# Performance work log

Hardware: AMD Instinct MI355X
Metric: run time of the kernel (lower is better)

The kernel has to match this reference:

```python
import jax, jax.numpy as jnp
import numpy as np

B, S, I, H, L1, O = 128, 1024, 256, 512, 256, 64

def _xavier(key, shape):
    fan_in, fan_out = shape[-2] if len(shape) > 1 else shape[-1], shape[-1]
    limit = float(np.sqrt(6.0 / (fan_in + fan_out)))
    return jax.random.uniform(key, shape, jnp.float32, -limit, limit)

def setup_inputs() -> dict:
    key = jax.random.key(0)
    ks = jax.random.split(key, 20)
    d = {"X": jax.random.normal(ks[0], (B, S, I), jnp.float32)}
    names = [("W_xi", (I, H)), ("W_hi", (H, H)), ("b_i", (1, H)),
             ("W_xf", (I, H)), ("W_hf", (H, H)), ("b_f", (1, H)),
             ("W_xo", (I, H)), ("W_ho", (H, H)), ("b_o", (1, H)),
             ("W_xc", (I, H)), ("W_hc", (H, H)), ("b_c", (1, H)),
             ("W_o1", (H, L1)), ("b_o1", (1, L1)), ("W_o2", (L1, O)), ("b_o2", (1, O))]
    for k, (n, shp) in zip(ks[1:], names):
        d[n] = _xavier(k, shp)
    return d

def reference(X, W_xi, W_hi, b_i, W_xf, W_hf, b_f, W_xo, W_ho, b_o, W_xc, W_hc, b_c, W_o1, b_o1, W_o2, b_o2):
    batch = X.shape[0]
    hid = W_hi.shape[0]
    # Precompute all input projections in one big GEMM: [B,S,4H]
    Wx = jnp.concatenate([W_xi, W_xf, W_xo, W_xc], axis=1)
    pre = jnp.einsum('bsi,ig->bsg', X, Wx)  # [B,S,4H]
    pre = jnp.transpose(pre, (1, 0, 2))     # [S,B,4H] for scan

    def step(carry, p):
        Hs, Cs = carry
        pi, pf, po, pc = jnp.split(p, 4, axis=-1)
        Ig = jax.nn.sigmoid(pi + Hs @ W_hi + b_i)
        Fg = jax.nn.sigmoid(pf + Hs @ W_hf + b_f)
        Og = jax.nn.sigmoid(po + Hs @ W_ho + b_o)
        Ct = jnp.tanh(pc + Hs @ W_hc + b_c)
        Cn = Fg * Cs + Ig * Ct
        # NOTE: original module uses tanh(C) + O (addition), not O * tanh(C)
        Hn = jnp.tanh(Cn) + Og
        return (Hn, Cn), None

    H0 = jnp.zeros((batch, hid), X.dtype)
    C0 = jnp.zeros((batch, hid), X.dtype)
    (Hf, Cf), _ = jax.lax.scan(step, (H0, C0), pre)
    # Output head: only the final timestep's output is returned by the loop
    h1 = jax.nn.relu(Hf @ W_o1 + b_o1)
    output = jax.nn.softmax(h1 @ W_o2 + b_o2, axis=1)
    return output, Hf, Cf
```

## Files before the change

kernel.cpp:

```cpp
#include <hip/hip_runtime.h>

#define B_   128
#define S_   1024
#define I_   256
#define H_   512
#define L1_  256
#define O_   64

#define NGRP 8
#define WGPG 32
#define MB   16
#define NH   16
#define NCOL 64
#define SX   8
#define SH   16

#define HB_UINTS_PER_BUF 32768

typedef __attribute__((ext_vector_type(8))) short short8;
typedef __attribute__((ext_vector_type(4))) float f4;
typedef __attribute__((ext_vector_type(4))) unsigned u32x4;

__device__ __forceinline__ unsigned short f2bf(float x) {
  unsigned u = __builtin_bit_cast(unsigned, x);
  u += 0x7FFFu + ((u >> 16) & 1u);
  return (unsigned short)(u >> 16);
}

__device__ __forceinline__ f4 mfma_bf16(short8 a, short8 b, f4 c) {
  asm("v_mfma_f32_16x16x32_bf16 %0, %1, %2, %0" : "+v"(c) : "v"(a), "v"(b));
  return c;
}

__global__ __launch_bounds__(256, 1)
void lstm_rec(const float* __restrict__ X,
              const float* __restrict__ Wxi, const float* __restrict__ Whi, const float* __restrict__ bi,
              const float* __restrict__ Wxf, const float* __restrict__ Whf, const float* __restrict__ bfp,
              const float* __restrict__ Wxo, const float* __restrict__ Who, const float* __restrict__ bop,
              const float* __restrict__ Wxc, const float* __restrict__ Whc, const float* __restrict__ bcp,
              float* __restrict__ out, unsigned* __restrict__ flags, unsigned* __restrict__ Hbuf)
{
  __shared__ unsigned short WhF[4][SH][64][8];
  __shared__ unsigned short WxF[4][SX][64][8];
  __shared__ unsigned short As[SX + SH][64][8];
  __shared__ float Ps[MB][NCOL];
  __shared__ float bias_s[NCOL];
  __shared__ int go_s;

  const int tid  = threadIdx.x;
  const int lane = tid & 63;
  const int wv   = tid >> 6;
  const int g    = blockIdx.x & 7;
  const int jg   = blockIdx.x >> 3;
  const int j0   = jg * NH;
  const int b0   = g * MB;

  const float* Whg[4] = {Whi, Whf, Who, Whc};
  const float* Wxg[4] = {Wxi, Wxf, Wxo, Wxc};
  const float* bg[4]  = {bi, bfp, bop, bcp};

  for (int gate = 0; gate < 4; ++gate) {
    const float* Wp = Whg[gate];
    for (int it = 0; it < 32; ++it) {
      int idx = it * 256 + tid;
      int k = idx >> 4, c = idx & 15;
      WhF[gate][k >> 5][((k & 31) >> 3) * 16 + c][k & 7] = f2bf(Wp[(size_t)k * H_ + j0 + c]);
    }
    const float* Xp = Wxg[gate];
    for (int it = 0; it < 16; ++it) {
      int idx = it * 256 + tid;
      int k = idx >> 4, c = idx & 15;
      WxF[gate][k >> 5][((k & 31) >> 3) * 16 + c][k & 7] = f2bf(Xp[(size_t)k * H_ + j0 + c]);
    }
  }
  if (tid < NCOL) bias_s[tid] = bg[tid >> 4][j0 + (tid & 15)];
  if (tid == 0) go_s = 0;
  __syncthreads();

  float Creg = 0.f;
  const int pb = tid >> 4;
  const int ph = tid & 15;
  unsigned* myflags = flags + g * 32;

  for (int t = 0; t < S_; ++t) {
    #pragma unroll
    for (int it = 0; it < 2; ++it) {
      int idx = it * 256 + tid;
      int s = idx >> 6, pos = idx & 63;
      int row = pos & 15, k0 = s * 32 + (pos >> 4) * 8;
      const float* src = X + ((size_t)(b0 + row) * S_ + t) * I_ + k0;
      float4 v0 = *(const float4*)(src);
      float4 v1 = *(const float4*)(src + 4);
      union { unsigned short us[8]; u32x4 v; } pk;
      pk.us[0] = f2bf(v0.x); pk.us[1] = f2bf(v0.y); pk.us[2] = f2bf(v0.z); pk.us[3] = f2bf(v0.w);
      pk.us[4] = f2bf(v1.x); pk.us[5] = f2bf(v1.y); pk.us[6] = f2bf(v1.z); pk.us[7] = f2bf(v1.w);
      *(u32x4*)&As[s][pos][0] = pk.v;
    }
    __syncthreads();

    float bv = bias_s[wv * 16 + (lane & 15)];
    f4 acc = {bv, bv, bv, bv};
    asm("s_nop 1" : "+v"(acc));
    #pragma unroll
    for (int s = 0; s < SX; ++s) {
      short8 a = *(const short8*)&As[s][lane][0];
      short8 b = *(const short8*)&WxF[wv][s][lane][0];
      acc = mfma_bf16(a, b, acc);
    }

    if (t > 0) {
      if (wv == 0) {
        const unsigned target = (unsigned)t;
        for (;;) {
          unsigned v = __hip_atomic_load(myflags + (lane & 31),
                                         __ATOMIC_RELAXED, __HIP_MEMORY_SCOPE_AGENT);
          if (__all(v >= target)) break;
          __builtin_amdgcn_s_sleep(1);
        }
        if (lane == 0) *(volatile int*)&go_s = t;
      } else {
        while (*(volatile int*)&go_s < t) __builtin_amdgcn_s_sleep(1);
      }
      const u32x4* gp = (const u32x4*)(Hbuf + (size_t)(t & 1) * HB_UINTS_PER_BUF + g * 4096);
      u32x4 r0, r1, r2, r3;
      asm volatile(
        "global_load_dwordx4 %0, %4, off sc0 sc1\n\t"
        "global_load_dwordx4 %1, %5, off sc0 sc1\n\t"
        "global_load_dwordx4 %2, %6, off sc0 sc1\n\t"
        "global_load_dwordx4 %3, %7, off sc0 sc1\n\t"
        "s_waitcnt vmcnt(0)"
        : "=&v"(r0), "=&v"(r1), "=&v"(r2), "=&v"(r3)
        : "v"(gp + tid), "v"(gp + tid + 256), "v"(gp + tid + 512), "v"(gp + tid + 768)
        : "memory");
      u32x4* lp = (u32x4*)&As[SX][0][0];
      lp[tid]       = r0;
      lp[tid + 256] = r1;
      lp[tid + 512] = r2;
      lp[tid + 768] = r3;
    }
    __syncthreads();

    if (t > 0) {
      #pragma unroll
      for (int s = 0; s < SH; ++s) {
        short8 a = *(const short8*)&As[SX + s][lane][0];
        short8 b = *(const short8*)&WhF[wv][s][lane][0];
        acc = mfma_bf16(a, b, acc);
      }
    }
    asm("s_nop 7\n\ts_nop 7" : "+v"(acc));
    {
      int col = wv * 16 + (lane & 15);
      int r0 = (lane >> 4) * 4;
      Ps[r0 + 0][col] = acc[0];
      Ps[r0 + 1][col] = acc[1];
      Ps[r0 + 2][col] = acc[2];
      Ps[r0 + 3][col] = acc[3];
    }
    __syncthreads();

    {
      float pi = Ps[pb][ph];
      float pf = Ps[pb][16 + ph];
      float po = Ps[pb][32 + ph];
      float pc = Ps[pb][48 + ph];
      float Ig = 1.f / (1.f + __expf(-pi));
      float Fg = 1.f / (1.f + __expf(-pf));
      float Og = 1.f / (1.f + __expf(-po));
      float Ct = 1.f - 2.f / (__expf(2.f * pc) + 1.f);
      float Cn = Fg * Creg + Ig * Ct;
      Creg = Cn;
      float Hn = (1.f - 2.f / (__expf(2.f * Cn) + 1.f)) + Og;
      if (t < S_ - 1) {
        unsigned hb = f2bf(Hn);
        unsigned other = (unsigned)__shfl_xor((int)hb, 1, 64);
        if ((ph & 1) == 0) {
          unsigned packed = hb | (other << 16);
          int sl = jg >> 1;
          int pos = ((jg & 1) * 2 + (ph >> 3)) * 16 + pb;
          unsigned* dst = Hbuf + (size_t)((t + 1) & 1) * HB_UINTS_PER_BUF + g * 4096
                        + (sl * 64 + pos) * 4 + ((ph & 7) >> 1);
          __hip_atomic_store(dst, packed, __ATOMIC_RELAXED, __HIP_MEMORY_SCOPE_AGENT);
        }
      } else {
        out[B_ * O_ + (size_t)(b0 + pb) * H_ + j0 + ph] = Hn;
        out[B_ * O_ + B_ * H_ + (size_t)(b0 + pb) * H_ + j0 + ph] = Cn;
      }
    }
    if (t < S_ - 1) {
      __syncthreads();
      if (tid == 0)
        __hip_atomic_store(myflags + jg, (unsigned)(t + 1),
                           __ATOMIC_RELAXED, __HIP_MEMORY_SCOPE_AGENT);
    }
  }
}

__global__ __launch_bounds__(256, 1)
void lstm_head(const float* __restrict__ Hf,
               const float* __restrict__ Wo1, const float* __restrict__ bo1,
               const float* __restrict__ Wo2, const float* __restrict__ bo2,
               float* __restrict__ outp)
{
  __shared__ float hf[H_];
  __shared__ float h1[L1_];
  const int tid = threadIdx.x;
  const int b = blockIdx.x;
  hf[tid]       = Hf[(size_t)b * H_ + tid];
  hf[tid + 256] = Hf[(size_t)b * H_ + tid + 256];
  __syncthreads();
  float a = bo1[tid];
  #pragma unroll 8
  for (int k = 0; k < H_; ++k) a = fmaf(hf[k], Wo1[(size_t)k * L1_ + tid], a);
  h1[tid] = fmaxf(a, 0.f);
  __syncthreads();
  if (tid < O_) {
    float l = bo2[tid];
    #pragma unroll 8
    for (int j = 0; j < L1_; ++j) l = fmaf(h1[j], Wo2[(size_t)j * O_ + tid], l);
    float m = l;
    #pragma unroll
    for (int off = 32; off > 0; off >>= 1) m = fmaxf(m, __shfl_xor(m, off, 64));
    float e = __expf(l - m);
    float ssum = e;
    #pragma unroll
    for (int off = 32; off > 0; off >>= 1) ssum += __shfl_xor(ssum, off, 64);
    outp[(size_t)b * O_ + tid] = e / ssum;
  }
}

extern "C" void kernel_launch(void* const* d_in, const int* in_sizes, int n_in,
                              void* d_out, int out_size, void* d_ws, size_t ws_size,
                              hipStream_t stream) {
  (void)in_sizes; (void)n_in; (void)out_size; (void)ws_size;
  const float* X   = (const float*)d_in[0];
  const float* Wxi = (const float*)d_in[1];
  const float* Whi = (const float*)d_in[2];
  const float* bi  = (const float*)d_in[3];
  const float* Wxf = (const float*)d_in[4];
  const float* Whf = (const float*)d_in[5];
  const float* bfv = (const float*)d_in[6];
  const float* Wxo = (const float*)d_in[7];
  const float* Who = (const float*)d_in[8];
  const float* bo  = (const float*)d_in[9];
  const float* Wxc = (const float*)d_in[10];
  const float* Whc = (const float*)d_in[11];
  const float* bc  = (const float*)d_in[12];
  const float* Wo1 = (const float*)d_in[13];
  const float* bo1 = (const float*)d_in[14];
  const float* Wo2 = (const float*)d_in[15];
  const float* bo2 = (const float*)d_in[16];
  float* out = (float*)d_out;

  unsigned* flags = (unsigned*)d_ws;
  unsigned* Hbuf  = (unsigned*)((char*)d_ws + 1024);

  hipMemsetAsync(d_ws, 0, 1024, stream);
  hipLaunchKernelGGL(lstm_rec, dim3(NGRP * WGPG), dim3(256), 0, stream,
                     X, Wxi, Whi, bi, Wxf, Whf, bfv, Wxo, Who, bo, Wxc, Whc, bc,
                     out, flags, Hbuf);
  hipLaunchKernelGGL(lstm_head, dim3(B_), dim3(256), 0, stream,
                     out + B_ * O_, Wo1, bo1, Wo2, bo2, out);
}
```

Measured before the change: 2.703 ms.

## Prefetch next X step, keep weights in registers, pick XCC-local cache scope

The X slice for step t+1 is now loaded into registers during step t and written to a double-buffered LDS area that reuses the WxF storage, taking the X load latency off the critical path. The Wx and Wh MFMA operand fragments are also held in registers, so the per-step LDS reads of weights go away. A startup handshake records each workgroup's XCC ID. When all workgroups in a batch group share one XCC, the H exchange uses sc0-only loads and stores so it can stay in the local L2 rather than going to system scope. The flag poll is issued early, before the Wx MFMAs, to hide its latency. The costs are much higher register pressure, extra startup synchronisation, and reliance on same-XCC coherence being correct.

```diff
diff --git a/kernel.cpp b/kernel.cpp
--- a/kernel.cpp
+++ b/kernel.cpp
@@ -38,14 +38,16 @@
               const float* __restrict__ Wxf, const float* __restrict__ Whf, const float* __restrict__ bfp,
               const float* __restrict__ Wxo, const float* __restrict__ Who, const float* __restrict__ bop,
               const float* __restrict__ Wxc, const float* __restrict__ Whc, const float* __restrict__ bcp,
-              float* __restrict__ out, unsigned* __restrict__ flags, unsigned* __restrict__ Hbuf)
+              float* __restrict__ out, unsigned* __restrict__ flags,
+              unsigned* __restrict__ xslots, unsigned* __restrict__ Hbuf)
 {
   __shared__ unsigned short WhF[4][SH][64][8];
   __shared__ unsigned short WxF[4][SX][64][8];
-  __shared__ unsigned short As[SX + SH][64][8];
+  __shared__ unsigned short AsH[SH][64][8];
   __shared__ float Ps[MB][NCOL];
   __shared__ float bias_s[NCOL];
   __shared__ int go_s;
+  __shared__ int mode_s;
 
   const int tid  = threadIdx.x;
   const int lane = tid & 63;
@@ -55,6 +57,25 @@
   const int j0   = jg * NH;
   const int b0   = g * MB;
 
+  unsigned xcc;
+  asm volatile("s_getreg_b32 %0, hwreg(HW_REG_XCC_ID)" : "=s"(xcc));
+  xcc &= 15u;
+  if (tid == 0)
+    __hip_atomic_store(xslots + g * 32 + jg, xcc + 1u,
+                       __ATOMIC_RELAXED, __HIP_MEMORY_SCOPE_AGENT);
+
+  const int idxA = tid, idxB = 256 + tid;
+  const int sA = idxA >> 6, posA = idxA & 63;
+  const int sB = idxB >> 6, posB = idxB & 63;
+  const int offA = (sA * 64 + posA) * 8;
+  const int offB = (sB * 64 + posB) * 8;
+  const float* bpa = X + (size_t)(b0 + (posA & 15)) * S_ * I_ + (sA * 32 + (posA >> 4) * 8);
+  const float* bpb = X + (size_t)(b0 + (posB & 15)) * S_ * I_ + (sB * 32 + (posB >> 4) * 8);
+  float4 ra0 = *(const float4*)(bpa);
+  float4 ra1 = *(const float4*)(bpa + 4);
+  float4 rb0 = *(const float4*)(bpb);
+  float4 rb1 = *(const float4*)(bpb + 4);
+
   const float* Whg[4] = {Whi, Whf, Who, Whc};
   const float* Wxg[4] = {Wxi, Wxf, Wxo, Wxc};
   const float* bg[4]  = {bi, bfp, bop, bcp};
@@ -77,62 +98,103 @@
   if (tid == 0) go_s = 0;
   __syncthreads();
 
+  short8 wx[SX], wh[SH];
+  #pragma unroll
+  for (int s = 0; s < SX; ++s) wx[s] = *(const short8*)&WxF[wv][s][lane][0];
+  #pragma unroll
+  for (int s = 0; s < SH; ++s) wh[s] = *(const short8*)&WhF[wv][s][lane][0];
+
+  if (wv == 0) {
+    unsigned v;
+    for (;;) {
+      v = __hip_atomic_load(xslots + g * 32 + (lane & 31),
+                            __ATOMIC_RELAXED, __HIP_MEMORY_SCOPE_AGENT);
+      if (__all((int)(v != 0u))) break;
+      __builtin_amdgcn_s_sleep(1);
+    }
+    unsigned f0 = (unsigned)__shfl((int)v, 0, 64);
+    int same = __all((int)(v == f0));
+    if (lane == 0) mode_s = same;
+  }
+  __syncthreads();
+  const bool l2m = (mode_s != 0);
+
+  unsigned short* axbase = &WxF[0][0][0][0];
+  const int AXSTRIDE = SX * 64 * 8;
+  {
+    union { unsigned short us[8]; u32x4 v; } pk;
+    pk.us[0]=f2bf(ra0.x); pk.us[1]=f2bf(ra0.y); pk.us[2]=f2bf(ra0.z); pk.us[3]=f2bf(ra0.w);
+    pk.us[4]=f2bf(ra1.x); pk.us[5]=f2bf(ra1.y); pk.us[6]=f2bf(ra1.z); pk.us[7]=f2bf(ra1.w);
+    *(u32x4*)(axbase + offA) = pk.v;
+    pk.us[0]=f2bf(rb0.x); pk.us[1]=f2bf(rb0.y); pk.us[2]=f2bf(rb0.z); pk.us[3]=f2bf(rb0.w);
+    pk.us[4]=f2bf(rb1.x); pk.us[5]=f2bf(rb1.y); pk.us[6]=f2bf(rb1.z); pk.us[7]=f2bf(rb1.w);
+    *(u32x4*)(axbase + offB) = pk.v;
+  }
+  __syncthreads();
+
   float Creg = 0.f;
   const int pb = tid >> 4;
   const int ph = tid & 15;
   unsigned* myflags = flags + g * 32;
 
   for (int t = 0; t < S_; ++t) {
-    #pragma unroll
-    for (int it = 0; it < 2; ++it) {
-      int idx = it * 256 + tid;
-      int s = idx >> 6, pos = idx & 63;
-      int row = pos & 15, k0 = s * 32 + (pos >> 4) * 8;
-      const float* src = X + ((size_t)(b0 + row) * S_ + t) * I_ + k0;
-      float4 v0 = *(const float4*)(src);
-      float4 v1 = *(const float4*)(src + 4);
-      union { unsigned short us[8]; u32x4 v; } pk;
-      pk.us[0] = f2bf(v0.x); pk.us[1] = f2bf(v0.y); pk.us[2] = f2bf(v0.z); pk.us[3] = f2bf(v0.w);
-      pk.us[4] = f2bf(v1.x); pk.us[5] = f2bf(v1.y); pk.us[6] = f2bf(v1.z); pk.us[7] = f2bf(v1.w);
-      *(u32x4*)&As[s][pos][0] = pk.v;
-    }
-    __syncthreads();
+    const bool last = (t == S_ - 1);
+
+    unsigned fpre = 0u;
+    const unsigned* fp0 = myflags + (lane & 31);
+    if (t > 0 && wv == 0)
+      asm volatile("global_load_dword %0, %1, off sc0 sc1"
+                   : "+v"(fpre) : "v"(fp0) : "memory");
 
     float bv = bias_s[wv * 16 + (lane & 15)];
     f4 acc = {bv, bv, bv, bv};
     asm("s_nop 1" : "+v"(acc));
+    const unsigned short* ax = axbase + (t & 1) * AXSTRIDE;
     #pragma unroll
     for (int s = 0; s < SX; ++s) {
-      short8 a = *(const short8*)&As[s][lane][0];
-      short8 b = *(const short8*)&WxF[wv][s][lane][0];
-      acc = mfma_bf16(a, b, acc);
+      short8 a = *(const short8*)(ax + (s * 64 + lane) * 8);
+      acc = mfma_bf16(a, wx[s], acc);
     }
 
     if (t > 0) {
       if (wv == 0) {
-        const unsigned target = (unsigned)t;
-        for (;;) {
-          unsigned v = __hip_atomic_load(myflags + (lane & 31),
-                                         __ATOMIC_RELAXED, __HIP_MEMORY_SCOPE_AGENT);
-          if (__all(v >= target)) break;
-          __builtin_amdgcn_s_sleep(1);
+        asm volatile("s_waitcnt vmcnt(0)" : "+v"(fpre) :: "memory");
+        __builtin_amdgcn_sched_barrier(0);
+        if (!__all((int)(fpre >= (unsigned)t))) {
+          for (;;) {
+            unsigned v = __hip_atomic_load(fp0, __ATOMIC_RELAXED, __HIP_MEMORY_SCOPE_AGENT);
+            if (__all((int)(v >= (unsigned)t))) break;
+            __builtin_amdgcn_s_sleep(1);
+          }
         }
-        if (lane == 0) *(volatile int*)&go_s = t;
+        if (lane == 0) *(volatile int*)&go_s = (int)t;
       } else {
-        while (*(volatile int*)&go_s < t) __builtin_amdgcn_s_sleep(1);
+        while (*(volatile int*)&go_s < (int)t) __builtin_amdgcn_s_sleep(1);
       }
       const u32x4* gp = (const u32x4*)(Hbuf + (size_t)(t & 1) * HB_UINTS_PER_BUF + g * 4096);
       u32x4 r0, r1, r2, r3;
-      asm volatile(
-        "global_load_dwordx4 %0, %4, off sc0 sc1\n\t"
-        "global_load_dwordx4 %1, %5, off sc0 sc1\n\t"
-        "global_load_dwordx4 %2, %6, off sc0 sc1\n\t"
-        "global_load_dwordx4 %3, %7, off sc0 sc1\n\t"
-        "s_waitcnt vmcnt(0)"
-        : "=&v"(r0), "=&v"(r1), "=&v"(r2), "=&v"(r3)
-        : "v"(gp + tid), "v"(gp + tid + 256), "v"(gp + tid + 512), "v"(gp + tid + 768)
-        : "memory");
-      u32x4* lp = (u32x4*)&As[SX][0][0];
+      if (l2m) {
+        asm volatile(
+          "global_load_dwordx4 %0, %4, off sc0\n\t"
+          "global_load_dwordx4 %1, %5, off sc0\n\t"
+          "global_load_dwordx4 %2, %6, off sc0\n\t"
+          "global_load_dwordx4 %3, %7, off sc0\n\t"
+          "s_waitcnt vmcnt(0)"
+          : "=&v"(r0), "=&v"(r1), "=&v"(r2), "=&v"(r3)
+          : "v"(gp + tid), "v"(gp + tid + 256), "v"(gp + tid + 512), "v"(gp + tid + 768)
+          : "memory");
+      } else {
+        asm volatile(
+          "global_load_dwordx4 %0, %4, off sc0 sc1\n\t"
+          "global_load_dwordx4 %1, %5, off sc0 sc1\n\t"
+          "global_load_dwordx4 %2, %6, off sc0 sc1\n\t"
+          "global_load_dwordx4 %3, %7, off sc0 sc1\n\t"
+          "s_waitcnt vmcnt(0)"
+          : "=&v"(r0), "=&v"(r1), "=&v"(r2), "=&v"(r3)
+          : "v"(gp + tid), "v"(gp + tid + 256), "v"(gp + tid + 512), "v"(gp + tid + 768)
+          : "memory");
+      }
+      u32x4* lp = (u32x4*)&AsH[0][0][0];
       lp[tid]       = r0;
       lp[tid + 256] = r1;
       lp[tid + 512] = r2;
@@ -140,22 +202,30 @@
     }
     __syncthreads();
 
+    if (!last) {
+      const float* pa = bpa + (size_t)(t + 1) * I_;
+      const float* pb2 = bpb + (size_t)(t + 1) * I_;
+      ra0 = *(const float4*)(pa);
+      ra1 = *(const float4*)(pa + 4);
+      rb0 = *(const float4*)(pb2);
+      rb1 = *(const float4*)(pb2 + 4);
+    }
+
     if (t > 0) {
       #pragma unroll
       for (int s = 0; s < SH; ++s) {
-        short8 a = *(const short8*)&As[SX + s][lane][0];
-        short8 b = *(const short8*)&WhF[wv][s][lane][0];
-        acc = mfma_bf16(a, b, acc);
+        short8 a = *(const short8*)&AsH[s][lane][0];
+        acc = mfma_bf16(a, wh[s], acc);
       }
     }
     asm("s_nop 7\n\ts_nop 7" : "+v"(acc));
     {
       int col = wv * 16 + (lane & 15);
-      int r0 = (lane >> 4) * 4;
-      Ps[r0 + 0][col] = acc[0];
-      Ps[r0 + 1][col] = acc[1];
-      Ps[r0 + 2][col] = acc[2];
-      Ps[r0 + 3][col] = acc[3];
+      int r0i = (lane >> 4) * 4;
+      Ps[r0i + 0][col] = acc[0];
+      Ps[r0i + 1][col] = acc[1];
+      Ps[r0i + 2][col] = acc[2];
+      Ps[r0i + 3][col] = acc[3];
     }
     __syncthreads();
 
@@ -171,7 +241,7 @@
       float Cn = Fg * Creg + Ig * Ct;
       Creg = Cn;
       float Hn = (1.f - 2.f / (__expf(2.f * Cn) + 1.f)) + Og;
-      if (t < S_ - 1) {
+      if (!last) {
         unsigned hb = f2bf(Hn);
         unsigned other = (unsigned)__shfl_xor((int)hb, 1, 64);
         if ((ph & 1) == 0) {
@@ -180,14 +250,26 @@
           int pos = ((jg & 1) * 2 + (ph >> 3)) * 16 + pb;
           unsigned* dst = Hbuf + (size_t)((t + 1) & 1) * HB_UINTS_PER_BUF + g * 4096
                         + (sl * 64 + pos) * 4 + ((ph & 7) >> 1);
-          __hip_atomic_store(dst, packed, __ATOMIC_RELAXED, __HIP_MEMORY_SCOPE_AGENT);
+          if (l2m)
+            asm volatile("global_store_dword %0, %1, off sc0" :: "v"(dst), "v"(packed) : "memory");
+          else
+            asm volatile("global_store_dword %0, %1, off sc0 sc1" :: "v"(dst), "v"(packed) : "memory");
         }
       } else {
         out[B_ * O_ + (size_t)(b0 + pb) * H_ + j0 + ph] = Hn;
         out[B_ * O_ + B_ * H_ + (size_t)(b0 + pb) * H_ + j0 + ph] = Cn;
       }
     }
-    if (t < S_ - 1) {
+    if (!last) {
+      unsigned short* axw = axbase + ((t + 1) & 1) * AXSTRIDE;
+      union { unsigned short us[8]; u32x4 v; } pk;
+      pk.us[0]=f2bf(ra0.x); pk.us[1]=f2bf(ra0.y); pk.us[2]=f2bf(ra0.z); pk.us[3]=f2bf(ra0.w);
+      pk.us[4]=f2bf(ra1.x); pk.us[5]=f2bf(ra1.y); pk.us[6]=f2bf(ra1.z); pk.us[7]=f2bf(ra1.w);
+      *(u32x4*)(axw + offA) = pk.v;
+      pk.us[0]=f2bf(rb0.x); pk.us[1]=f2bf(rb0.y); pk.us[2]=f2bf(rb0.z); pk.us[3]=f2bf(rb0.w);
+      pk.us[4]=f2bf(rb1.x); pk.us[5]=f2bf(rb1.y); pk.us[6]=f2bf(rb1.z); pk.us[7]=f2bf(rb1.w);
+      *(u32x4*)(axw + offB) = pk.v;
+
       __syncthreads();
       if (tid == 0)
         __hip_atomic_store(myflags + jg, (unsigned)(t + 1),
@@ -252,13 +334,14 @@
   const float* bo2 = (const float*)d_in[16];
   float* out = (float*)d_out;
 
-  unsigned* flags = (unsigned*)d_ws;
-  unsigned* Hbuf  = (unsigned*)((char*)d_ws + 1024);
-
-  hipMemsetAsync(d_ws, 0, 1024, stream);
+  unsigned* flags  = (unsigned*)d_ws;
+  unsigned* xslots = (unsigned*)((char*)d_ws + 1024);
+  unsigned* Hbuf   = (unsigned*)((char*)d_ws + 2048);
+
+  hipMemsetAsync(d_ws, 0, 2048, stream);
   hipLaunchKernelGGL(lstm_rec, dim3(NGRP * WGPG), dim3(256), 0, stream,
                      X, Wxi, Whi, bi, Wxf, Whf, bfv, Wxo, Who, bo, Wxc, Whc, bc,
-                     out, flags, Hbuf);
+                     out, flags, xslots, Hbuf);
   hipLaunchKernelGGL(lstm_head, dim3(B_), dim3(256), 0, stream,
                      out + B_ * O_, Wo1, bo1, Wo2, bo2, out);
 }
```

Result: faster. 2.292 ms (-15.2%).
